# Performance work log

Hardware: AMD Instinct MI355X
Metric: run time of the kernel (lower is better)

Reference implementation:

```python
import jax, jax.numpy as jnp
import numpy as np

BETA = 0.25
EPS = 1e-12

def normalise(x):
    # L2 normalise over last axis
    return x / jnp.sqrt(jnp.sum(x * x, axis=-1, keepdims=True) + EPS)

def setup_inputs() -> dict:
    key = jax.random.key(0)
    k = jax.random.split(key, 6)
    N, d, c, P = 8192, 768, 256, 16384
    return {
        "z": jax.random.normal(k[0], (N, d), dtype=jnp.float32),
        "W_in": jax.random.normal(k[1], (d, c), dtype=jnp.float32) * 0.02,
        "b_in": jnp.zeros((c,), dtype=jnp.float32),
        "W_out": jax.random.normal(k[2], (c, d), dtype=jnp.float32) * 0.02,
        "b_out": jnp.zeros((d,), dtype=jnp.float32),
        "codebook": jax.random.normal(k[3], (P, c), dtype=jnp.float32),
    }

def reference(z, W_in, b_in, W_out, b_out, codebook):
    sg = jax.lax.stop_gradient
    # input projection + L2 normalise
    zq = normalise(z @ W_in + b_in)                 # [N, c]
    cb = normalise(codebook)                        # [P, c]
    # squared euclidean distances: ||z||^2 - 2 z.c + ||c||^2
    dist = (jnp.sum(zq * zq, axis=-1, keepdims=True)
            - 2.0 * jnp.einsum('nc,pc->np', zq, cb)
            + jnp.sum(cb * cb, axis=-1)[None, :])   # [N, P]
    idxes = jnp.argmin(dist, axis=-1)               # [N]
    codes = normalise(codebook[idxes])              # gather + normalise, [N, c]
    loss = BETA * (zq - sg(codes)) ** 2 + (sg(zq) - codes) ** 2
    # straight-through estimator
    codes = zq + sg(codes - zq)
    out = codes @ W_out + b_out                     # [N, d]
    return out, loss, idxes
```

## Files before the change

kernel.cpp:

```cpp
#include <hip/hip_runtime.h>
#include <hip/hip_fp16.h>
#include <math.h>

#define NN 8192
#define DD 768
#define CC 256
#define PP 16384
#define NG 256
#define MARGIN 5.0e-3f
#define BETA_C 1.25f
#define EPS_C 1e-12f

typedef __attribute__((ext_vector_type(8))) _Float16 f16x8;
typedef __attribute__((ext_vector_type(4))) float f32x4;
typedef __attribute__((ext_vector_type(16))) float f32x16;

static __device__ __forceinline__ ushort f2h(float x) {
    _Float16 h = (_Float16)x;
    return __builtin_bit_cast(unsigned short, h);
}

static __device__ __forceinline__ void gload_lds16(const void* g, void* l) {
    __builtin_amdgcn_global_load_lds(
        (const __attribute__((address_space(1))) unsigned int*)g,
        (__attribute__((address_space(3))) unsigned int*)l, 16, 0, 0);
}

__global__ __launch_bounds__(256) void k_gemm_in(const float* __restrict__ z,
    const float* __restrict__ W, const float* __restrict__ b,
    float* __restrict__ zq)
{
    __shared__ float zt[64][36];
    __shared__ float wt[32][68];
    const int t = threadIdx.x;
    const int ti = t >> 4, tj = t & 15;
    const int n0 = blockIdx.x * 64;
    const int c0 = blockIdx.y * 64;

    f32x4 acc[4];
#pragma unroll
    for (int r = 0; r < 4; ++r) acc[r] = (f32x4){0.f, 0.f, 0.f, 0.f};

    for (int k0 = 0; k0 < DD; k0 += 32) {
        __syncthreads();
#pragma unroll
        for (int l = 0; l < 2; ++l) {
            int idx = l * 256 + t;
            int row = idx >> 3, c4 = idx & 7;
            *reinterpret_cast<float4*>(&zt[row][c4 * 4]) =
                *reinterpret_cast<const float4*>(&z[(size_t)(n0 + row) * DD + k0 + c4 * 4]);
            int krow = idx >> 4, w4 = idx & 15;
            *reinterpret_cast<float4*>(&wt[krow][w4 * 4]) =
                *reinterpret_cast<const float4*>(&W[(size_t)(k0 + krow) * CC + c0 + w4 * 4]);
        }
        __syncthreads();
#pragma unroll
        for (int kk = 0; kk < 32; kk += 4) {
            float4 a4[4], b4[4];
#pragma unroll
            for (int r = 0; r < 4; ++r)
                a4[r] = *reinterpret_cast<const float4*>(&zt[ti * 4 + r][kk]);
#pragma unroll
            for (int q = 0; q < 4; ++q)
                b4[q] = *reinterpret_cast<const float4*>(&wt[kk + q][tj * 4]);
#pragma unroll
            for (int q = 0; q < 4; ++q)
#pragma unroll
                for (int r = 0; r < 4; ++r) {
                    float av = ((const float*)&a4[r])[q];
                    acc[r].x += av * b4[q].x;
                    acc[r].y += av * b4[q].y;
                    acc[r].z += av * b4[q].z;
                    acc[r].w += av * b4[q].w;
                }
        }
    }
#pragma unroll
    for (int r = 0; r < 4; ++r) {
        int col = c0 + tj * 4;
        float4 o;
        o.x = acc[r].x + b[col];
        o.y = acc[r].y + b[col + 1];
        o.z = acc[r].z + b[col + 2];
        o.w = acc[r].w + b[col + 3];
        *reinterpret_cast<float4*>(&zq[(size_t)(n0 + ti * 4 + r) * CC + col]) = o;
    }
}

__global__ __launch_bounds__(256) void k_norm2(const float* __restrict__ src,
    float* __restrict__ dstf32, ushort* __restrict__ dsth,
    float* __restrict__ sq, float* __restrict__ rinvout, int rows)
{
    const int wave = threadIdx.x >> 6;
    const int lane = threadIdx.x & 63;
    const int row = blockIdx.x * 4 + wave;
    if (row >= rows) return;
    float4 v = *reinterpret_cast<const float4*>(&src[(size_t)row * CC + lane * 4]);
    float s = v.x * v.x + v.y * v.y + v.z * v.z + v.w * v.w;
#pragma unroll
    for (int off = 32; off; off >>= 1) s += __shfl_xor(s, off, 64);
    float r = 1.0f / sqrtf(s + EPS_C);
    v.x *= r; v.y *= r; v.z *= r; v.w *= r;
    if (dstf32)
        *reinterpret_cast<float4*>(&dstf32[(size_t)row * CC + lane * 4]) = v;
    ushort4 hv;
    hv.x = f2h(v.x); hv.y = f2h(v.y); hv.z = f2h(v.z); hv.w = f2h(v.w);
    *reinterpret_cast<ushort4*>(&dsth[(size_t)row * CC + lane * 4]) = hv;
    if (sq) {
        float s2 = v.x * v.x + v.y * v.y + v.z * v.z + v.w * v.w;
#pragma unroll
        for (int off = 32; off; off >>= 1) s2 += __shfl_xor(s2, off, 64);
        if (lane == 0) {
            sq[row] = s2;
            if (rinvout) rinvout[row] = r;
        }
    }
}

__global__ __launch_bounds__(256) void k_dist(
    const ushort* __restrict__ cbh, const ushort* __restrict__ zqh,
    const float* __restrict__ cz2,
    float* __restrict__ gmin, unsigned long long* __restrict__ maskA)
{
    __shared__ ushort lA[128 * 64];
    __shared__ ushort lB[128 * 64];
    const int t = threadIdx.x;
    const int lane = t & 63;
    const int w = t >> 6;
    const int wr = w >> 1;
    const int wc = w & 1;
    const int p0 = blockIdx.x * 128;
    const int n0 = blockIdx.y * 128;
    const int kh = lane >> 5;
    const int r31 = lane & 31;

    const int pb = p0 + wr * 64;
    f32x16 acc[2][2];
#pragma unroll
    for (int mi = 0; mi < 2; ++mi)
#pragma unroll
        for (int q = 0; q < 4; ++q) {
            float4 cz = *reinterpret_cast<const float4*>(
                &cz2[pb + mi * 32 + q * 8 + kh * 4]);
#pragma unroll
            for (int j = 0; j < 4; ++j) {
                float v = -0.5f * ((const float*)&cz.x)[j];
                acc[mi][0][q * 4 + j] = v;
                acc[mi][1][q * 4 + j] = v;
            }
        }

    const int srow = lane >> 3;
    const int schunk = (lane & 7) ^ srow;
    const char* srcA = (const char*)cbh + (size_t)(p0 + w * 32 + srow) * (CC * 2) + schunk * 16;
    const char* srcB = (const char*)zqh + (size_t)(n0 + w * 32 + srow) * (CC * 2) + schunk * 16;
    char* dstA = (char*)lA + (w * 32) * 128;
    char* dstB = (char*)lB + (w * 32) * 128;

    const char* lAc = (const char*)lA;
    const char* lBc = (const char*)lB;
    const int arow = wr * 64 + r31;
    const int brow = wc * 64 + r31;
    const int sx = (r31 & 7) << 4;

    for (int k0 = 0; k0 < CC; k0 += 64) {
        __syncthreads();
#pragma unroll
        for (int i = 0; i < 4; ++i) {
            gload_lds16(srcA + (size_t)i * 8 * (CC * 2) + k0 * 2, dstA + i * 1024);
            gload_lds16(srcB + (size_t)i * 8 * (CC * 2) + k0 * 2, dstB + i * 1024);
        }
        __syncthreads();
#pragma unroll
        for (int ks = 0; ks < 4; ++ks) {
            const int ko = ((ks * 32 + kh * 16) ^ sx);
            f16x8 a0 = *reinterpret_cast<const f16x8*>(lAc + arow * 128 + ko);
            f16x8 a1 = *reinterpret_cast<const f16x8*>(lAc + (arow + 32) * 128 + ko);
            f16x8 b0 = *reinterpret_cast<const f16x8*>(lBc + brow * 128 + ko);
            f16x8 b1 = *reinterpret_cast<const f16x8*>(lBc + (brow + 32) * 128 + ko);
            acc[0][0] = __builtin_amdgcn_mfma_f32_32x32x16_f16(a0, b0, acc[0][0], 0, 0, 0);
            acc[0][1] = __builtin_amdgcn_mfma_f32_32x32x16_f16(a0, b1, acc[0][1], 0, 0, 0);
            acc[1][0] = __builtin_amdgcn_mfma_f32_32x32x16_f16(a1, b0, acc[1][0], 0, 0, 0);
            acc[1][1] = __builtin_amdgcn_mfma_f32_32x32x16_f16(a1, b1, acc[1][1], 0, 0, 0);
        }
    }

    const int grp = (p0 >> 6) + wr;
#pragma unroll
    for (int ni = 0; ni < 2; ++ni) {
        float M = -1e30f;
#pragma unroll
        for (int mi = 0; mi < 2; ++mi)
#pragma unroll
            for (int r = 0; r < 16; ++r) M = fmaxf(M, acc[mi][ni][r]);
        M = fmaxf(M, __shfl_xor(M, 32, 64));
        const float thr = M - 0.5f * MARGIN;
        unsigned long long msk = 0ull;
#pragma unroll
        for (int mi = 0; mi < 2; ++mi)
#pragma unroll
            for (int q = 0; q < 4; ++q) {
                unsigned nib = 0u;
#pragma unroll
                for (int j = 0; j < 4; ++j)
                    nib |= (acc[mi][ni][q * 4 + j] >= thr) ? (1u << j) : 0u;
                msk |= (unsigned long long)nib << (mi * 32 + q * 8 + kh * 4);
            }
        msk |= __shfl_xor(msk, 32, 64);
        if (kh == 0) {
            int n = n0 + wc * 64 + ni * 32 + r31;
            gmin[(size_t)n * NG + grp] = -2.0f * M;
            maskA[(size_t)n * NG + grp] = msk;
        }
    }
}

__global__ __launch_bounds__(256) void k_pick(
    const float* __restrict__ gmin, const unsigned long long* __restrict__ maskA,
    const float* __restrict__ zqn, const float* __restrict__ cb_raw,
    const float* __restrict__ rinv, const float* __restrict__ cz2,
    float* __restrict__ idxf, int* __restrict__ idxi)
{
    __shared__ int lst[4][256];
    __shared__ int cnt[4];
    const int t = threadIdx.x;
    const int w = t >> 6;
    const int lane = t & 63;
    const int row = blockIdx.x * 4 + w;

    float4 zr = *reinterpret_cast<const float4*>(&zqn[(size_t)row * CC + lane * 4]);
    float4 gv = *reinterpret_cast<const float4*>(&gmin[(size_t)row * NG + lane * 4]);

    float pm = fminf(fminf(gv.x, gv.y), fminf(gv.z, gv.w));
#pragma unroll
    for (int off = 1; off < 64; off <<= 1) pm = fminf(pm, __shfl_xor(pm, off, 64));
    const float thresh = pm + MARGIN;

    if (lane == 0) cnt[w] = 0;
    __syncthreads();
    {
        const float g4[4] = {gv.x, gv.y, gv.z, gv.w};
#pragma unroll
        for (int j = 0; j < 4; ++j)
            if (g4[j] <= thresh) {
                int pos = atomicAdd(&cnt[w], 1);
                lst[w][pos] = lane * 4 + j;
            }
    }
    __syncthreads();

    const int nc = cnt[w];
    unsigned long long best = ~0ull;
    for (int ci = 0; ci < nc; ++ci) {
        int g = lst[w][ci];
        unsigned long long msk = maskA[(size_t)row * NG + g];
        while (msk) {
            int bit = __ffsll((long long)msk) - 1;
            msk &= msk - 1;
            int p = g * 64 + bit;
            float rv = rinv[p];
            float4 c4 = *reinterpret_cast<const float4*>(&cb_raw[(size_t)p * CC + lane * 4]);
            float part = (c4.x * rv) * zr.x + (c4.y * rv) * zr.y
                       + (c4.z * rv) * zr.z + (c4.w * rv) * zr.w;
#pragma unroll
            for (int off = 1; off < 64; off <<= 1) part += __shfl_xor(part, off, 64);
            float d4 = fmaf(-2.0f, part, 4.0f + cz2[p]);
            unsigned long long pk = ((unsigned long long)__float_as_uint(d4) << 32) | (unsigned)p;
            best = best < pk ? best : pk;
        }
    }
    if (lane == 0) {
        int p = (int)(best & 0xffffffffu);
        idxf[row] = (float)p;
        idxi[row] = p;
    }
}

__global__ __launch_bounds__(256) void k_codes(const float* __restrict__ zqn,
    const float* __restrict__ cb_raw, const float* __restrict__ rinv,
    const int* __restrict__ idxv, float* __restrict__ codes,
    float* __restrict__ loss)
{
    int idx = blockIdx.x * 256 + threadIdx.x;
    int n = idx >> 6;
    int c4 = idx & 63;
    int p = idxv[n];
    float rv = rinv[p];
    float4 cv = *reinterpret_cast<const float4*>(&cb_raw[(size_t)p * CC + c4 * 4]);
    cv.x *= rv; cv.y *= rv; cv.z *= rv; cv.w *= rv;
    *reinterpret_cast<float4*>(&codes[(size_t)n * CC + c4 * 4]) = cv;
    float4 zv = *reinterpret_cast<const float4*>(&zqn[(size_t)n * CC + c4 * 4]);
    float4 lv;
    float dx = zv.x - cv.x, dy = zv.y - cv.y, dz = zv.z - cv.z, dw = zv.w - cv.w;
    lv.x = BETA_C * dx * dx; lv.y = BETA_C * dy * dy;
    lv.z = BETA_C * dz * dz; lv.w = BETA_C * dw * dw;
    *reinterpret_cast<float4*>(&loss[(size_t)n * CC + c4 * 4]) = lv;
}

__global__ __launch_bounds__(256) void k_gemm_out(const float* __restrict__ A,
    const float* __restrict__ W, const float* __restrict__ b,
    float* __restrict__ out)
{
    __shared__ float at[64][36];
    __shared__ float wt[32][68];
    const int t = threadIdx.x;
    const int ti = t >> 4, tj = t & 15;
    const int n0 = blockIdx.x * 64;
    const int c0 = blockIdx.y * 64;

    f32x4 acc[4];
#pragma unroll
    for (int r = 0; r < 4; ++r) acc[r] = (f32x4){0.f, 0.f, 0.f, 0.f};

    for (int k0 = 0; k0 < CC; k0 += 32) {
        __syncthreads();
#pragma unroll
        for (int l = 0; l < 2; ++l) {
            int idx = l * 256 + t;
            int row = idx >> 3, c4 = idx & 7;
            *reinterpret_cast<float4*>(&at[row][c4 * 4]) =
                *reinterpret_cast<const float4*>(&A[(size_t)(n0 + row) * CC + k0 + c4 * 4]);
            int krow = idx >> 4, w4 = idx & 15;
            *reinterpret_cast<float4*>(&wt[krow][w4 * 4]) =
                *reinterpret_cast<const float4*>(&W[(size_t)(k0 + krow) * DD + c0 + w4 * 4]);
        }
        __syncthreads();
#pragma unroll
        for (int kk = 0; kk < 32; kk += 4) {
            float4 a4[4], b4[4];
#pragma unroll
            for (int r = 0; r < 4; ++r)
                a4[r] = *reinterpret_cast<const float4*>(&at[ti * 4 + r][kk]);
#pragma unroll
            for (int q = 0; q < 4; ++q)
                b4[q] = *reinterpret_cast<const float4*>(&wt[kk + q][tj * 4]);
#pragma unroll
            for (int q = 0; q < 4; ++q)
#pragma unroll
                for (int r = 0; r < 4; ++r) {
                    float av = ((const float*)&a4[r])[q];
                    acc[r].x += av * b4[q].x;
                    acc[r].y += av * b4[q].y;
                    acc[r].z += av * b4[q].z;
                    acc[r].w += av * b4[q].w;
                }
        }
    }
#pragma unroll
    for (int r = 0; r < 4; ++r) {
        int col = c0 + tj * 4;
        float4 o;
        o.x = acc[r].x + b[col];
        o.y = acc[r].y + b[col + 1];
        o.z = acc[r].z + b[col + 2];
        o.w = acc[r].w + b[col + 3];
        *reinterpret_cast<float4*>(&out[(size_t)(n0 + ti * 4 + r) * DD + col]) = o;
    }
}

extern "C" void kernel_launch(void* const* d_in, const int* in_sizes, int n_in,
                              void* d_out, int out_size, void* d_ws, size_t ws_size,
                              hipStream_t stream)
{
    const float* z        = (const float*)d_in[0];
    const float* W_in     = (const float*)d_in[1];
    const float* b_in     = (const float*)d_in[2];
    const float* W_out    = (const float*)d_in[3];
    const float* b_out    = (const float*)d_in[4];
    const float* codebook = (const float*)d_in[5];

    char* ws = (char*)d_ws;
    ushort* zqh   = (ushort*)(ws);
    ushort* cbh   = (ushort*)(ws + 4194304);
    float*  codes = (float*)(ws + 12582912);
    float*  cz2   = (float*)(ws + 20971520);
    float*  rinv  = (float*)(ws + 21037056);
    int*    idxi  = (int*)  (ws + 21102592);

    float* out  = (float*)d_out;
    float* loss = out + (size_t)NN * DD;
    float* idxf = loss + (size_t)NN * CC;

    float* gmin = (float*)d_out;
    unsigned long long* maskA = (unsigned long long*)((char*)d_out + 8388608);
    float* zq = loss;

    k_gemm_in<<<dim3(NN / 64, CC / 64), 256, 0, stream>>>(z, W_in, b_in, zq);
    k_norm2<<<NN / 4, 256, 0, stream>>>(zq, zq, zqh, (float*)nullptr, (float*)nullptr, NN);
    k_norm2<<<PP / 4, 256, 0, stream>>>(codebook, (float*)nullptr, cbh, cz2, rinv, PP);
    k_dist<<<dim3(PP / 128, NN / 128), 256, 0, stream>>>(cbh, zqh, cz2, gmin, maskA);
    k_pick<<<NN / 4, 256, 0, stream>>>(gmin, maskA, zq, codebook, rinv, cz2, idxf, idxi);
    k_codes<<<(NN * CC / 4) / 256, 256, 0, stream>>>(zq, codebook, rinv, idxi, codes, loss);
    k_gemm_out<<<dim3(NN / 64, DD / 64), 256, 0, stream>>>(codes, W_out, b_out, out);
}
```

Baseline: 214.2 us.

## Move output GEMM to split-bf16 MFMA and enlarge distance kernel tile

Replaces the scalar fp32 output projection with an MFMA kernel that splits codes and W_out into bf16 hi/lo parts and accumulates three products, approximating fp32 accuracy on matrix cores. A new kernel transposes W_out and splits it, and k_codes now writes bf16 hi/lo codes instead of fp32. Separately, the distance kernel tile grows from 128 to 256 codebook rows per block, raising operand reuse at the cost of more registers and LDS. The split-bf16 scheme adds three MFMAs per tile and an extra launch, and its output rounding differs slightly from the fp32 version.

```diff
diff --git a/kernel.cpp b/kernel.cpp
--- a/kernel.cpp
+++ b/kernel.cpp
@@ -12,12 +12,20 @@
 #define EPS_C 1e-12f
 
 typedef __attribute__((ext_vector_type(8))) _Float16 f16x8;
+typedef __attribute__((ext_vector_type(8))) short bf16x8;
 typedef __attribute__((ext_vector_type(4))) float f32x4;
 typedef __attribute__((ext_vector_type(16))) float f32x16;
 
 static __device__ __forceinline__ ushort f2h(float x) {
     _Float16 h = (_Float16)x;
     return __builtin_bit_cast(unsigned short, h);
+}
+static __device__ __forceinline__ ushort f2bf(float x) {
+    unsigned u = __float_as_uint(x);
+    return (ushort)((u + 0x7fffu + ((u >> 16) & 1u)) >> 16);
+}
+static __device__ __forceinline__ float bf2f(ushort h) {
+    return __uint_as_float(((unsigned)h) << 16);
 }
 
 static __device__ __forceinline__ void gload_lds16(const void* g, void* l) {
@@ -117,31 +125,57 @@
     }
 }
 
+__global__ __launch_bounds__(256) void k_split_w(const float* __restrict__ W,
+    ushort* __restrict__ wthi, ushort* __restrict__ wtlo)
+{
+    __shared__ float tile[64][68];
+    const int t = threadIdx.x;
+    const int d0 = blockIdx.x * 64;
+    const int k0 = blockIdx.y * 64;
+#pragma unroll
+    for (int i = 0; i < 16; ++i) {
+        int row = i * 4 + (t >> 6);
+        int col = t & 63;
+        tile[row][col] = W[(size_t)(k0 + row) * DD + d0 + col];
+    }
+    __syncthreads();
+#pragma unroll
+    for (int i = 0; i < 16; ++i) {
+        int drow = i * 4 + (t >> 6);
+        int kc = t & 63;
+        float v = tile[kc][drow];
+        ushort hi = f2bf(v);
+        float rres = v - bf2f(hi);
+        ushort lo = f2bf(rres);
+        wthi[(size_t)(d0 + drow) * CC + k0 + kc] = hi;
+        wtlo[(size_t)(d0 + drow) * CC + k0 + kc] = lo;
+    }
+}
+
 __global__ __launch_bounds__(256) void k_dist(
     const ushort* __restrict__ cbh, const ushort* __restrict__ zqh,
     const float* __restrict__ cz2,
     float* __restrict__ gmin, unsigned long long* __restrict__ maskA)
 {
-    __shared__ ushort lA[128 * 64];
+    __shared__ ushort lA[256 * 64];
     __shared__ ushort lB[128 * 64];
     const int t = threadIdx.x;
     const int lane = t & 63;
     const int w = t >> 6;
     const int wr = w >> 1;
     const int wc = w & 1;
-    const int p0 = blockIdx.x * 128;
+    const int p0 = blockIdx.x * 256;
     const int n0 = blockIdx.y * 128;
     const int kh = lane >> 5;
     const int r31 = lane & 31;
 
-    const int pb = p0 + wr * 64;
-    f32x16 acc[2][2];
-#pragma unroll
-    for (int mi = 0; mi < 2; ++mi)
+    f32x16 acc[4][2];
+#pragma unroll
+    for (int mi = 0; mi < 4; ++mi) {
+        const int pbm = p0 + wr * 128 + mi * 32;
 #pragma unroll
         for (int q = 0; q < 4; ++q) {
-            float4 cz = *reinterpret_cast<const float4*>(
-                &cz2[pb + mi * 32 + q * 8 + kh * 4]);
+            float4 cz = *reinterpret_cast<const float4*>(&cz2[pbm + q * 8 + kh * 4]);
 #pragma unroll
             for (int j = 0; j < 4; ++j) {
                 float v = -0.5f * ((const float*)&cz.x)[j];
@@ -149,68 +183,78 @@
                 acc[mi][1][q * 4 + j] = v;
             }
         }
+    }
 
     const int srow = lane >> 3;
     const int schunk = (lane & 7) ^ srow;
-    const char* srcA = (const char*)cbh + (size_t)(p0 + w * 32 + srow) * (CC * 2) + schunk * 16;
+    const char* srcA = (const char*)cbh + (size_t)(p0 + w * 64 + srow) * (CC * 2) + schunk * 16;
     const char* srcB = (const char*)zqh + (size_t)(n0 + w * 32 + srow) * (CC * 2) + schunk * 16;
-    char* dstA = (char*)lA + (w * 32) * 128;
+    char* dstA = (char*)lA + (w * 64) * 128;
     char* dstB = (char*)lB + (w * 32) * 128;
 
     const char* lAc = (const char*)lA;
     const char* lBc = (const char*)lB;
-    const int arow = wr * 64 + r31;
-    const int brow = wc * 64 + r31;
     const int sx = (r31 & 7) << 4;
 
     for (int k0 = 0; k0 < CC; k0 += 64) {
         __syncthreads();
 #pragma unroll
-        for (int i = 0; i < 4; ++i) {
+        for (int i = 0; i < 8; ++i)
             gload_lds16(srcA + (size_t)i * 8 * (CC * 2) + k0 * 2, dstA + i * 1024);
+#pragma unroll
+        for (int i = 0; i < 4; ++i)
             gload_lds16(srcB + (size_t)i * 8 * (CC * 2) + k0 * 2, dstB + i * 1024);
-        }
         __syncthreads();
 #pragma unroll
         for (int ks = 0; ks < 4; ++ks) {
             const int ko = ((ks * 32 + kh * 16) ^ sx);
-            f16x8 a0 = *reinterpret_cast<const f16x8*>(lAc + arow * 128 + ko);
-            f16x8 a1 = *reinterpret_cast<const f16x8*>(lAc + (arow + 32) * 128 + ko);
-            f16x8 b0 = *reinterpret_cast<const f16x8*>(lBc + brow * 128 + ko);
-            f16x8 b1 = *reinterpret_cast<const f16x8*>(lBc + (brow + 32) * 128 + ko);
-            acc[0][0] = __builtin_amdgcn_mfma_f32_32x32x16_f16(a0, b0, acc[0][0], 0, 0, 0);
-            acc[0][1] = __builtin_amdgcn_mfma_f32_32x32x16_f16(a0, b1, acc[0][1], 0, 0, 0);
-            acc[1][0] = __builtin_amdgcn_mfma_f32_32x32x16_f16(a1, b0, acc[1][0], 0, 0, 0);
-            acc[1][1] = __builtin_amdgcn_mfma_f32_32x32x16_f16(a1, b1, acc[1][1], 0, 0, 0);
-        }
-    }
-
-    const int grp = (p0 >> 6) + wr;
+            f16x8 af[4], bfv[2];
+#pragma unroll
+            for (int mi = 0; mi < 4; ++mi)
+                af[mi] = *reinterpret_cast<const f16x8*>(
+                    lAc + (wr * 128 + mi * 32 + r31) * 128 + ko);
+#pragma unroll
+            for (int ni = 0; ni < 2; ++ni)
+                bfv[ni] = *reinterpret_cast<const f16x8*>(
+                    lBc + (wc * 64 + ni * 32 + r31) * 128 + ko);
+#pragma unroll
+            for (int mi = 0; mi < 4; ++mi)
+#pragma unroll
+                for (int ni = 0; ni < 2; ++ni)
+                    acc[mi][ni] = __builtin_amdgcn_mfma_f32_32x32x16_f16(
+                        af[mi], bfv[ni], acc[mi][ni], 0, 0, 0);
+        }
+    }
+
 #pragma unroll
     for (int ni = 0; ni < 2; ++ni) {
-        float M = -1e30f;
-#pragma unroll
-        for (int mi = 0; mi < 2; ++mi)
-#pragma unroll
-            for (int r = 0; r < 16; ++r) M = fmaxf(M, acc[mi][ni][r]);
-        M = fmaxf(M, __shfl_xor(M, 32, 64));
-        const float thr = M - 0.5f * MARGIN;
-        unsigned long long msk = 0ull;
-#pragma unroll
-        for (int mi = 0; mi < 2; ++mi)
-#pragma unroll
-            for (int q = 0; q < 4; ++q) {
-                unsigned nib = 0u;
-#pragma unroll
-                for (int j = 0; j < 4; ++j)
-                    nib |= (acc[mi][ni][q * 4 + j] >= thr) ? (1u << j) : 0u;
-                msk |= (unsigned long long)nib << (mi * 32 + q * 8 + kh * 4);
+#pragma unroll
+        for (int g = 0; g < 2; ++g) {
+            float M = -1e30f;
+#pragma unroll
+            for (int m2 = 0; m2 < 2; ++m2)
+#pragma unroll
+                for (int r = 0; r < 16; ++r) M = fmaxf(M, acc[g * 2 + m2][ni][r]);
+            M = fmaxf(M, __shfl_xor(M, 32, 64));
+            const float thr = M - 0.5f * MARGIN;
+            unsigned long long msk = 0ull;
+#pragma unroll
+            for (int m2 = 0; m2 < 2; ++m2)
+#pragma unroll
+                for (int q = 0; q < 4; ++q) {
+                    unsigned nib = 0u;
+#pragma unroll
+                    for (int j = 0; j < 4; ++j)
+                        nib |= (acc[g * 2 + m2][ni][q * 4 + j] >= thr) ? (1u << j) : 0u;
+                    msk |= (unsigned long long)nib << (m2 * 32 + q * 8 + kh * 4);
+                }
+            msk |= __shfl_xor(msk, 32, 64);
+            if (kh == 0) {
+                int n = n0 + wc * 64 + ni * 32 + r31;
+                int grp = (p0 >> 6) + wr * 2 + g;
+                gmin[(size_t)n * NG + grp] = -2.0f * M;
+                maskA[(size_t)n * NG + grp] = msk;
             }
-        msk |= __shfl_xor(msk, 32, 64);
-        if (kh == 0) {
-            int n = n0 + wc * 64 + ni * 32 + r31;
-            gmin[(size_t)n * NG + grp] = -2.0f * M;
-            maskA[(size_t)n * NG + grp] = msk;
         }
     }
 }
@@ -278,8 +322,8 @@
 
 __global__ __launch_bounds__(256) void k_codes(const float* __restrict__ zqn,
     const float* __restrict__ cb_raw, const float* __restrict__ rinv,
-    const int* __restrict__ idxv, float* __restrict__ codes,
-    float* __restrict__ loss)
+    const int* __restrict__ idxv, ushort* __restrict__ chi,
+    ushort* __restrict__ clo, float* __restrict__ loss)
 {
     int idx = blockIdx.x * 256 + threadIdx.x;
     int n = idx >> 6;
@@ -288,73 +332,122 @@
     float rv = rinv[p];
     float4 cv = *reinterpret_cast<const float4*>(&cb_raw[(size_t)p * CC + c4 * 4]);
     cv.x *= rv; cv.y *= rv; cv.z *= rv; cv.w *= rv;
-    *reinterpret_cast<float4*>(&codes[(size_t)n * CC + c4 * 4]) = cv;
+    ushort4 hv, lv16;
+    {
+        hv.x = f2bf(cv.x); lv16.x = f2bf(cv.x - bf2f(hv.x));
+        hv.y = f2bf(cv.y); lv16.y = f2bf(cv.y - bf2f(hv.y));
+        hv.z = f2bf(cv.z); lv16.z = f2bf(cv.z - bf2f(hv.z));
+        hv.w = f2bf(cv.w); lv16.w = f2bf(cv.w - bf2f(hv.w));
+    }
+    *reinterpret_cast<ushort4*>(&chi[(size_t)n * CC + c4 * 4]) = hv;
+    *reinterpret_cast<ushort4*>(&clo[(size_t)n * CC + c4 * 4]) = lv16;
     float4 zv = *reinterpret_cast<const float4*>(&zqn[(size_t)n * CC + c4 * 4]);
-    float4 lv;
+    float4 lsv;
     float dx = zv.x - cv.x, dy = zv.y - cv.y, dz = zv.z - cv.z, dw = zv.w - cv.w;
-    lv.x = BETA_C * dx * dx; lv.y = BETA_C * dy * dy;
-    lv.z = BETA_C * dz * dz; lv.w = BETA_C * dw * dw;
-    *reinterpret_cast<float4*>(&loss[(size_t)n * CC + c4 * 4]) = lv;
-}
-
-__global__ __launch_bounds__(256) void k_gemm_out(const float* __restrict__ A,
-    const float* __restrict__ W, const float* __restrict__ b,
-    float* __restrict__ out)
-{
-    __shared__ float at[64][36];
-    __shared__ float wt[32][68];
+    lsv.x = BETA_C * dx * dx; lsv.y = BETA_C * dy * dy;
+    lsv.z = BETA_C * dz * dz; lsv.w = BETA_C * dw * dw;
+    *reinterpret_cast<float4*>(&loss[(size_t)n * CC + c4 * 4]) = lsv;
+}
+
+__global__ __launch_bounds__(256) void k_gemm_out_mfma(
+    const ushort* __restrict__ chi, const ushort* __restrict__ clo,
+    const ushort* __restrict__ wthi, const ushort* __restrict__ wtlo,
+    const float* __restrict__ bout, float* __restrict__ out)
+{
+    __shared__ ushort sAh[128 * 64];
+    __shared__ ushort sAl[128 * 64];
+    __shared__ ushort sBh[128 * 64];
+    __shared__ ushort sBl[128 * 64];
     const int t = threadIdx.x;
-    const int ti = t >> 4, tj = t & 15;
-    const int n0 = blockIdx.x * 64;
-    const int c0 = blockIdx.y * 64;
-
-    f32x4 acc[4];
-#pragma unroll
-    for (int r = 0; r < 4; ++r) acc[r] = (f32x4){0.f, 0.f, 0.f, 0.f};
-
-    for (int k0 = 0; k0 < CC; k0 += 32) {
-        __syncthreads();
-#pragma unroll
-        for (int l = 0; l < 2; ++l) {
-            int idx = l * 256 + t;
-            int row = idx >> 3, c4 = idx & 7;
-            *reinterpret_cast<float4*>(&at[row][c4 * 4]) =
-                *reinterpret_cast<const float4*>(&A[(size_t)(n0 + row) * CC + k0 + c4 * 4]);
-            int krow = idx >> 4, w4 = idx & 15;
-            *reinterpret_cast<float4*>(&wt[krow][w4 * 4]) =
-                *reinterpret_cast<const float4*>(&W[(size_t)(k0 + krow) * DD + c0 + w4 * 4]);
-        }
-        __syncthreads();
-#pragma unroll
-        for (int kk = 0; kk < 32; kk += 4) {
-            float4 a4[4], b4[4];
-#pragma unroll
-            for (int r = 0; r < 4; ++r)
-                a4[r] = *reinterpret_cast<const float4*>(&at[ti * 4 + r][kk]);
+    const int lane = t & 63;
+    const int w = t >> 6;
+    const int wr = w >> 1;
+    const int wc = w & 1;
+    const int nb = blockIdx.x * 128;
+    const int db = blockIdx.y * 128;
+    const int kh = lane >> 5;
+    const int r31 = lane & 31;
+
+    f32x16 acc[2][2];
+#pragma unroll
+    for (int mi = 0; mi < 2; ++mi)
+#pragma unroll
+        for (int ni = 0; ni < 2; ++ni)
+#pragma unroll
+            for (int r = 0; r < 16; ++r) acc[mi][ni][r] = 0.f;
+
+    const int srow = lane >> 3;
+    const int schunk = (lane & 7) ^ srow;
+    const size_t rowA = (size_t)(nb + w * 32 + srow) * CC;
+    const size_t rowB = (size_t)(db + w * 32 + srow) * CC;
+    const char* sAhsrc = (const char*)chi + rowA * 2 + schunk * 16;
+    const char* sAlsrc = (const char*)clo + rowA * 2 + schunk * 16;
+    const char* sBhsrc = (const char*)wthi + rowB * 2 + schunk * 16;
+    const char* sBlsrc = (const char*)wtlo + rowB * 2 + schunk * 16;
+    char* dA = (char*)sAh + (w * 32) * 128;
+    char* dAl = (char*)sAl + (w * 32) * 128;
+    char* dB = (char*)sBh + (w * 32) * 128;
+    char* dBl = (char*)sBl + (w * 32) * 128;
+
+    const int sx = (r31 & 7) << 4;
+
+    for (int k0 = 0; k0 < CC; k0 += 64) {
+        __syncthreads();
+#pragma unroll
+        for (int i = 0; i < 4; ++i) {
+            gload_lds16(sAhsrc + (size_t)i * 8 * (CC * 2) + k0 * 2, dA + i * 1024);
+            gload_lds16(sAlsrc + (size_t)i * 8 * (CC * 2) + k0 * 2, dAl + i * 1024);
+            gload_lds16(sBhsrc + (size_t)i * 8 * (CC * 2) + k0 * 2, dB + i * 1024);
+            gload_lds16(sBlsrc + (size_t)i * 8 * (CC * 2) + k0 * 2, dBl + i * 1024);
+        }
+        __syncthreads();
+#pragma unroll
+        for (int ks = 0; ks < 4; ++ks) {
+            const int ko = ((ks * 32 + kh * 16) ^ sx);
+            bf16x8 ah[2], al[2], bh[2], bl[2];
+#pragma unroll
+            for (int mi = 0; mi < 2; ++mi) {
+                ah[mi] = *reinterpret_cast<const bf16x8*>(
+                    (const char*)sAh + (wr * 64 + mi * 32 + r31) * 128 + ko);
+                al[mi] = *reinterpret_cast<const bf16x8*>(
+                    (const char*)sAl + (wr * 64 + mi * 32 + r31) * 128 + ko);
+            }
+#pragma unroll
+            for (int ni = 0; ni < 2; ++ni) {
+                bh[ni] = *reinterpret_cast<const bf16x8*>(
+                    (const char*)sBh + (wc * 64 + ni * 32 + r31) * 128 + ko);
+                bl[ni] = *reinterpret_cast<const bf16x8*>(
+                    (const char*)sBl + (wc * 64 + ni * 32 + r31) * 128 + ko);
+            }
+#pragma unroll
+            for (int mi = 0; mi < 2; ++mi)
+#pragma unroll
+                for (int ni = 0; ni < 2; ++ni) {
+                    acc[mi][ni] = __builtin_amdgcn_mfma_f32_32x32x16_bf16(
+                        ah[mi], bh[ni], acc[mi][ni], 0, 0, 0);
+                    acc[mi][ni] = __builtin_amdgcn_mfma_f32_32x32x16_bf16(
+                        ah[mi], bl[ni], acc[mi][ni], 0, 0, 0);
+                    acc[mi][ni] = __builtin_amdgcn_mfma_f32_32x32x16_bf16(
+                        al[mi], bh[ni], acc[mi][ni], 0, 0, 0);
+                }
+        }
+    }
+
+#pragma unroll
+    for (int ni = 0; ni < 2; ++ni) {
+        const int d = db + wc * 64 + ni * 32 + r31;
+        const float bv = bout[d];
+#pragma unroll
+        for (int mi = 0; mi < 2; ++mi) {
+            const int nbase = nb + wr * 64 + mi * 32 + 4 * kh;
 #pragma unroll
             for (int q = 0; q < 4; ++q)
-                b4[q] = *reinterpret_cast<const float4*>(&wt[kk + q][tj * 4]);
-#pragma unroll
-            for (int q = 0; q < 4; ++q)
-#pragma unroll
-                for (int r = 0; r < 4; ++r) {
-                    float av = ((const float*)&a4[r])[q];
-                    acc[r].x += av * b4[q].x;
-                    acc[r].y += av * b4[q].y;
-                    acc[r].z += av * b4[q].z;
-                    acc[r].w += av * b4[q].w;
+#pragma unroll
+                for (int j = 0; j < 4; ++j) {
+                    int n = nbase + j + 8 * q;
+                    out[(size_t)n * DD + d] = acc[mi][ni][q * 4 + j] + bv;
                 }
         }
-    }
-#pragma unroll
-    for (int r = 0; r < 4; ++r) {
-        int col = c0 + tj * 4;
-        float4 o;
-        o.x = acc[r].x + b[col];
-        o.y = acc[r].y + b[col + 1];
-        o.z = acc[r].z + b[col + 2];
-        o.w = acc[r].w + b[col + 3];
-        *reinterpret_cast<float4*>(&out[(size_t)(n0 + ti * 4 + r) * DD + col]) = o;
     }
 }
 
@@ -372,10 +465,13 @@
     char* ws = (char*)d_ws;
     ushort* zqh   = (ushort*)(ws);
     ushort* cbh   = (ushort*)(ws + 4194304);
-    float*  codes = (float*)(ws + 12582912);
-    float*  cz2   = (float*)(ws + 20971520);
-    float*  rinv  = (float*)(ws + 21037056);
-    int*    idxi  = (int*)  (ws + 21102592);
+    ushort* chi   = (ushort*)(ws + 12582912);
+    ushort* clo   = (ushort*)(ws + 16777216);
+    ushort* wthi  = (ushort*)(ws + 20971520);
+    ushort* wtlo  = (ushort*)(ws + 21364736);
+    float*  cz2   = (float*)(ws + 21757952);
+    float*  rinv  = (float*)(ws + 21823488);
+    int*    idxi  = (int*)  (ws + 21889024);
 
     float* out  = (float*)d_out;
     float* loss = out + (size_t)NN * DD;
@@ -388,8 +484,9 @@
     k_gemm_in<<<dim3(NN / 64, CC / 64), 256, 0, stream>>>(z, W_in, b_in, zq);
     k_norm2<<<NN / 4, 256, 0, stream>>>(zq, zq, zqh, (float*)nullptr, (float*)nullptr, NN);
     k_norm2<<<PP / 4, 256, 0, stream>>>(codebook, (float*)nullptr, cbh, cz2, rinv, PP);
-    k_dist<<<dim3(PP / 128, NN / 128), 256, 0, stream>>>(cbh, zqh, cz2, gmin, maskA);
+    k_split_w<<<dim3(DD / 64, CC / 64), 256, 0, stream>>>(W_out, wthi, wtlo);
+    k_dist<<<dim3(PP / 256, NN / 128), 256, 0, stream>>>(cbh, zqh, cz2, gmin, maskA);
     k_pick<<<NN / 4, 256, 0, stream>>>(gmin, maskA, zq, codebook, rinv, cz2, idxf, idxi);
-    k_codes<<<(NN * CC / 4) / 256, 256, 0, stream>>>(zq, codebook, rinv, idxi, codes, loss);
-    k_gemm_out<<<dim3(NN / 64, DD / 64), 256, 0, stream>>>(codes, W_out, b_out, out);
-}
+    k_codes<<<(NN * CC / 4) / 256, 256, 0, stream>>>(zq, codebook, rinv, idxi, chi, clo, loss);
+    k_gemm_out_mfma<<<dim3(NN / 128, DD / 128), 256, 0, stream>>>(chi, clo, wthi, wtlo, b_out, out);
+}
```

Result: faster. 183.2 us (-14.5%).
